# Optimization experiments

Hardware: AMD Instinct MI355X
Metric: run time of the kernel (lower is better)

## Reference

```python
import jax, jax.numpy as jnp
import numpy as np

B, S, HID = 2, 2048, 2048
H, HKV, D = 16, 8, 128
RQ, RK, RV = 6, 2, 2
WINDOW = 1024
SOFTCAP = 50.0
SCALING = D ** -0.5
NEG_INF = -2.3819763e38  # gemma mask fill value (fp32 safe)


def _rope(x, cos, sin):
    # Gemma rotary: split last dim into two halves treated as (real, imag).
    d2 = x.shape[-1] // 2
    x1, x2 = x[..., :d2], x[..., d2:]
    return jnp.concatenate([x1 * cos - x2 * sin, x1 * sin + x2 * cos], axis=-1)


def setup_inputs() -> dict:
    key = jax.random.key(0)
    ks = jax.random.split(key, 8)
    hidden_states = jax.random.normal(ks[0], (B, S, HID), jnp.float32)
    w = 0.02
    W_A_q = jax.random.normal(ks[1], (HID, H * RQ), jnp.float32) * w
    W_B_q = jax.random.normal(ks[2], (HID, H * RQ * D), jnp.float32) * w
    W_A_k = jax.random.normal(ks[3], (HID, HKV * RK), jnp.float32) * w
    W_B_k = jax.random.normal(ks[4], (HID, RK * D), jnp.float32) * w
    W_A_v = jax.random.normal(ks[5], (HID, HKV * RV), jnp.float32) * w
    W_B_v = jax.random.normal(ks[6], (HID, RV * D), jnp.float32) * w
    W_o = jax.random.normal(ks[7], (H * D, HID), jnp.float32) * w
    # rotary tables (theta=10000)
    pos = jnp.arange(S, dtype=jnp.float32)
    inv = 1.0 / (10000.0 ** (jnp.arange(0, D, 2, dtype=jnp.float32) / D))
    ang = pos[:, None] * inv[None, :]  # [S, D/2]
    freqs_cos, freqs_sin = jnp.cos(ang), jnp.sin(ang)
    # causal + sliding-window additive mask [B,1,S,S]
    i = jnp.arange(S)[:, None]
    j = jnp.arange(S)[None, :]
    allowed = (j <= i) & (i - j < WINDOW)
    mask = jnp.where(allowed, 0.0, NEG_INF).astype(jnp.float32)
    mask = jnp.broadcast_to(mask[None, None], (B, 1, S, S))
    kv_write_indices = jnp.arange(S, dtype=jnp.int32)  # prefill: identity write
    return {
        'hidden_states': hidden_states, 'W_A_q': W_A_q, 'W_B_q': W_B_q,
        'W_A_k': W_A_k, 'W_B_k': W_B_k, 'W_A_v': W_A_v, 'W_B_v': W_B_v,
        'W_o': W_o, 'freqs_cos': freqs_cos, 'freqs_sin': freqs_sin,
        'mask': mask, 'kv_write_indices': kv_write_indices,
    }


def reference(hidden_states, W_A_q, W_B_q, W_A_k, W_B_k, W_A_v, W_B_v, W_o,
              freqs_cos, freqs_sin, mask, kv_write_indices):
    # Prefill: kv_write_indices == arange(S); factorized cache == current factors.
    b, s, _ = hidden_states.shape
    Aq = (hidden_states @ W_A_q).reshape(b, s, H, RQ)       # [b,s,H,Rq]
    Bq = (hidden_states @ W_B_q).reshape(b, s, H, RQ, D)    # [b,s,H,Rq,d]
    Ak = (hidden_states @ W_A_k).reshape(b, s, HKV, RK)
    Bk = (hidden_states @ W_B_k).reshape(b, s, RK, D)
    Av = (hidden_states @ W_A_v).reshape(b, s, HKV, RV)
    Bv = (hidden_states @ W_B_v).reshape(b, s, RV, D)
    # RoPE on the B factors (as in the original: applied to B_q rows and B_k rows)
    Bq = _rope(Bq, freqs_cos[:, None, None, :], freqs_sin[:, None, None, :])
    Bk = _rope(Bk, freqs_cos[:, None, :], freqs_sin[:, None, :])
    # Contract rank factors. Identical math to the per-head
    # einsum('bqrd,bksd->bqkrs') + einsum('bqr,bks,bqkrs->bqk') since the
    # bilinear form factorizes: sum_{r,s} Aq_r Ak_s <Bq_r, Bk_s> = <q, k>.
    q = jnp.einsum('bshr,bshrd->bshd', Aq, Bq)               # [b,s,H,d]
    k = jnp.einsum('bsgr,bsrd->bsgd', Ak, Bk)                # [b,s,Hkv,d]
    v = jnp.einsum('bsgr,bsrd->bsgd', Av, Bv)
    rep = H // HKV
    k = jnp.repeat(k, rep, axis=2)                            # GQA expand
    v = jnp.repeat(v, rep, axis=2)
    scores = jnp.einsum('bqhd,bkhd->bhqk', q, k) * SCALING
    scores = jnp.tanh(scores / SOFTCAP) * SOFTCAP             # logit softcap
    scores = scores + mask                                    # local sliding mask
    probs = jax.nn.softmax(scores, axis=-1)
    out = jnp.einsum('bhqk,bkhd->bqhd', probs, v).reshape(b, s, H * D)
    return out @ W_o
```

## Files before the change

kernel.cpp:

```cpp
#include <hip/hip_runtime.h>
#include <hip/hip_bf16.h>

#define S_LEN 2048
#define HID 2048
#define NB 2
#define NH 16
#define NKV 8
#define DH 128
#define RQ 6
#define KG 2048
#define SCALING 0.08838834764831845f

typedef __attribute__((ext_vector_type(8))) short s16x8;
typedef __attribute__((ext_vector_type(4))) float f32x4;

__device__ __forceinline__ float bf2f(ushort u) {
    union { unsigned int i; float f; } v; v.i = ((unsigned int)u) << 16; return v.f;
}
__device__ __forceinline__ ushort f2bf(float f) {
    __hip_bfloat16 h = __float2bfloat16(f);
    return *reinterpret_cast<ushort*>(&h);
}
__device__ __forceinline__ void g2lds16(const void* g, void* l) {
    __builtin_amdgcn_global_load_lds((const __attribute__((address_space(1))) void*)g,
                                     (__attribute__((address_space(3))) void*)l, 16, 0, 0);
}

__global__ void k_prep(const float* __restrict__ hs, const float* __restrict__ WAq,
                       const float* __restrict__ WAk, const float* __restrict__ WAv,
                       const float* __restrict__ WBk, const float* __restrict__ WBv,
                       const float* __restrict__ WBq, const float* __restrict__ Wo,
                       ushort* __restrict__ Xb, ushort* __restrict__ WtS,
                       ushort* __restrict__ WtBq, ushort* __restrict__ WtWo) {
    __shared__ ushort tile[64][68];
    int idx = blockIdx.x;
    int t = threadIdx.x;
    if (idx < 2048) {
#pragma unroll
        for (int j = 0; j < 4; ++j) {
            int i = idx * 1024 + t + j * 256;
            float4 v = ((const float4*)hs)[i];
            ushort4 o;
            o.x = f2bf(v.x); o.y = f2bf(v.y); o.z = f2bf(v.z); o.w = f2bf(v.w);
            ((ushort4*)Xb)[i] = o;
        }
        return;
    }
    idx -= 2048;
    const float* in; ushort* out; int Nin, rowOff;
    if (idx < 64)        { in = WAq; out = WtS;  Nin = 96;    rowOff = 0; }
    else if (idx < 96)   { idx -= 64;   in = WAk; out = WtS;  Nin = 16;    rowOff = 96; }
    else if (idx < 128)  { idx -= 96;   in = WAv; out = WtS;  Nin = 16;    rowOff = 112; }
    else if (idx < 256)  { idx -= 128;  in = WBk; out = WtS;  Nin = 256;   rowOff = 128; }
    else if (idx < 384)  { idx -= 256;  in = WBv; out = WtS;  Nin = 256;   rowOff = 384; }
    else if (idx < 6528) { idx -= 384;  in = WBq; out = WtBq; Nin = 12288; rowOff = 0; }
    else                 { idx -= 6528; in = Wo;  out = WtWo; Nin = 2048;  rowOff = 0; }
    int k0 = (idx & 31) * 64, n0 = (idx >> 5) * 64;
#pragma unroll
    for (int i = 0; i < 4; ++i) {
        int f = t + i * 256;
        int r = f >> 4;
        int c = (f & 15) * 4;
        int nn = n0 + c;
        float4 v = make_float4(0.f, 0.f, 0.f, 0.f);
        if (nn < Nin) v = *(const float4*)&in[(size_t)(k0 + r) * Nin + nn];
        ushort4 u;
        u.x = f2bf(v.x); u.y = f2bf(v.y); u.z = f2bf(v.z); u.w = f2bf(v.w);
        *(ushort4*)&tile[r][c] = u;
    }
    __syncthreads();
#pragma unroll
    for (int i = 0; i < 4; ++i) {
        int f = t + i * 256;
        int nr = f >> 4;
        int kc = (f & 15) * 4;
        int nn = n0 + nr;
        if (nn < Nin) {
            ushort4 u;
            u.x = tile[kc][nr]; u.y = tile[kc + 1][nr];
            u.z = tile[kc + 2][nr]; u.w = tile[kc + 3][nr];
            *(ushort4*)&out[(size_t)(rowOff + nn) * KG + k0 + kc] = u;
        }
    }
}

__device__ __forceinline__ void stc(float* p, float v) { *p = v; }
__device__ __forceinline__ void stc(ushort* p, float v) { *p = f2bf(v); }

template<typename OutT>
__global__ __launch_bounds__(256, 2) void k_gemm(const ushort* __restrict__ A,
                                                 const ushort* __restrict__ Bt,
                                                 OutT* __restrict__ C, int ldc) {
    __shared__ ushort lA[128 * 64];
    __shared__ ushort lB[128 * 64];
    const int tid = threadIdx.x;
    const int l = tid & 63, w = tid >> 6;
    const int gx = gridDim.x;
    int flat = blockIdx.y * gx + blockIdx.x;
    const int nwg = gx * gridDim.y;
    if ((nwg & 7) == 0) {
        int qq = nwg >> 3;
        flat = (flat & 7) * qq + (flat >> 3);
    }
    const int m0 = (flat % gx) * 128, n0 = (flat / gx) * 128;
    const int wm = w >> 1, wn = w & 1;
    f32x4 acc[4][4] = {};
    const int swz = 16 * ((tid & 7) ^ ((tid >> 3) & 7));
    const int rowbase = tid >> 3;

    for (int k0 = 0; k0 < KG; k0 += 64) {
#pragma unroll
        for (int i = 0; i < 4; ++i) {
            int row = rowbase + i * 32;
            const char* srcA = (const char*)A + (((size_t)(m0 + row) * KG + k0) * 2) + swz;
            g2lds16(srcA, (char*)lA + tid * 16 + i * 4096);
            const char* srcB = (const char*)Bt + (((size_t)(n0 + row) * KG + k0) * 2) + swz;
            g2lds16(srcB, (char*)lB + tid * 16 + i * 4096);
        }
        __syncthreads();
#pragma unroll
        for (int kk = 0; kk < 2; ++kk) {
            s16x8 af[4], bfr[4];
            const int kb = kk * 64 + (l >> 4) * 16;
#pragma unroll
            for (int mf = 0; mf < 4; ++mf) {
                int row = wm * 64 + mf * 16 + (l & 15);
                af[mf] = *(const s16x8*)((const char*)lA + row * 128 + (kb ^ ((row & 7) << 4)));
            }
#pragma unroll
            for (int nf = 0; nf < 4; ++nf) {
                int row = wn * 64 + nf * 16 + (l & 15);
                bfr[nf] = *(const s16x8*)((const char*)lB + row * 128 + (kb ^ ((row & 7) << 4)));
            }
#pragma unroll
            for (int mf = 0; mf < 4; ++mf)
#pragma unroll
                for (int nf = 0; nf < 4; ++nf)
                    acc[mf][nf] = __builtin_amdgcn_mfma_f32_16x16x32_bf16(af[mf], bfr[nf], acc[mf][nf], 0, 0, 0);
        }
        __syncthreads();
    }
#pragma unroll
    for (int mf = 0; mf < 4; ++mf)
#pragma unroll
        for (int r = 0; r < 4; ++r) {
            int row = m0 + wm * 64 + mf * 16 + (l >> 4) * 4 + r;
#pragma unroll
            for (int nf = 0; nf < 4; ++nf) {
                int col = n0 + wn * 64 + nf * 16 + (l & 15);
                stc(C + (size_t)row * ldc + col, acc[mf][nf][r]);
            }
        }
}

__global__ __launch_bounds__(512, 2) void k_gemm8(const ushort* __restrict__ A,
                                                  const ushort* __restrict__ Bt,
                                                  ushort* __restrict__ C, int ldc) {
    __shared__ char sB[131072];
    const int tid = threadIdx.x;
    const int l = tid & 63, wid = tid >> 6;
    const int wr = wid >> 2, wc = wid & 3;

    int flat = blockIdx.x;
    const int nwg = gridDim.x;
    if ((nwg & 7) == 0) {
        int qq = nwg >> 3;
        flat = (flat & 7) * qq + (flat >> 3);
    }
    const int m0 = (flat & 15) * 256;
    const int n0 = (flat >> 4) * 256;

    const int rb = tid >> 3;
    const int swz = 16 * ((tid & 7) ^ (rb & 7));
    const char* pAh[2][2];
    const char* pBh[2][2];
#pragma unroll
    for (int h = 0; h < 2; ++h)
#pragma unroll
        for (int j = 0; j < 2; ++j) {
            pAh[h][j] = (const char*)A + (size_t)(m0 + j * 128 + h * 64 + rb) * (KG * 2) + swz;
            pBh[h][j] = (const char*)Bt + (size_t)(n0 + (j * 2 + (tid >> 8)) * 64 + h * 32 + (rb & 31)) * (KG * 2) + swz;
        }

    f32x4 acc[8][4] = {};
    s16x8 af[4][2], bf[4][2];

    const int arow = (l & 15) * 128;
    const int kxor0 = (0 * 64 + (l >> 4) * 16) ^ ((l & 7) << 4);
    const int kxor1 = (1 * 64 + (l >> 4) * 16) ^ ((l & 7) << 4);

#define STG_A(T, D, H)                                                                     \
    do {                                                                                   \
        g2lds16(pAh[H][0] + (size_t)(T) * 128, sB + (D) * 65536 + (H) * 16384 + tid * 16); \
        g2lds16(pAh[H][1] + (size_t)(T) * 128, sB + (D) * 65536 + (H) * 16384 + 8192 + tid * 16); \
    } while (0)
#define STG_B(T, D, H)                                                                     \
    do {                                                                                   \
        g2lds16(pBh[H][0] + (size_t)(T) * 128, sB + (D) * 65536 + 32768 + (H) * 16384 + tid * 16); \
        g2lds16(pBh[H][1] + (size_t)(T) * 128, sB + (D) * 65536 + 32768 + (H) * 16384 + 8192 + tid * 16); \
    } while (0)
#define RD_A(D, MH)                                                                        \
    do {                                                                                   \
        const char* ab = sB + (D) * 65536 + (MH) * 16384 + wr * 8192;                      \
        _Pragma("unroll") for (int mi = 0; mi < 4; ++mi) {                                 \
            af[mi][0] = *(const s16x8*)(ab + mi * 2048 + arow + kxor0);                    \
            af[mi][1] = *(const s16x8*)(ab + mi * 2048 + arow + kxor1);                    \
        }                                                                                  \
    } while (0)
#define RD_B(D, BH)                                                                        \
    do {                                                                                   \
        const char* bb = sB + (D) * 65536 + 32768 + (BH) * 16384 + wc * 4096;              \
        _Pragma("unroll") for (int ni = 0; ni < 2; ++ni) {                                 \
            bf[(BH) * 2 + ni][0] = *(const s16x8*)(bb + ni * 2048 + arow + kxor0);         \
            bf[(BH) * 2 + ni][1] = *(const s16x8*)(bb + ni * 2048 + arow + kxor1);         \
        }                                                                                  \
    } while (0)
#define QMFMA(MQ, NQ)                                                                      \
    do {                                                                                   \
        __builtin_amdgcn_s_setprio(1);                                                     \
        _Pragma("unroll") for (int mi = 0; mi < 4; ++mi)                                   \
        _Pragma("unroll") for (int ni = 0; ni < 2; ++ni)                                   \
        _Pragma("unroll") for (int k2 = 0; k2 < 2; ++k2)                                   \
            acc[(MQ) * 4 + mi][(NQ) * 2 + ni] = __builtin_amdgcn_mfma_f32_16x16x32_bf16(   \
                af[mi][k2], bf[(NQ) * 2 + ni][k2], acc[(MQ) * 4 + mi][(NQ) * 2 + ni], 0, 0, 0); \
        __builtin_amdgcn_s_setprio(0);                                                     \
    } while (0)
#define BAR()                                   \
    do {                                        \
        asm volatile("" ::: "memory");          \
        __builtin_amdgcn_s_barrier();           \
        asm volatile("" ::: "memory");          \
    } while (0)
#define VM6() asm volatile("s_waitcnt vmcnt(6)" ::: "memory")
#define VM0() asm volatile("s_waitcnt vmcnt(0)" ::: "memory")

    STG_A(0, 0, 0); STG_A(0, 0, 1); STG_B(0, 0, 0); STG_B(0, 0, 1);
    STG_B(1, 1, 0); STG_B(1, 1, 1); STG_A(1, 1, 0);
    VM6();
    BAR();

    for (int i = 0; i < 16; ++i) {
        const bool last = (i == 15);
        const int t1 = 2 * i + 1, t2 = 2 * i + 2, t3 = 2 * i + 3;
        RD_A(0, 0); RD_B(0, 0);
        STG_A(t1, 1, 1);
        BAR(); QMFMA(0, 0); BAR();
        RD_B(0, 1);
        if (!last) STG_A(t2, 0, 0);
        BAR(); QMFMA(0, 1); BAR();
        RD_A(0, 1);
        if (!last) STG_B(t2, 0, 0);
        BAR(); QMFMA(1, 1); BAR();
        if (!last) { STG_B(t2, 0, 1); VM6(); } else { VM0(); }
        BAR(); QMFMA(1, 0); BAR();
        RD_A(1, 0); RD_B(1, 0);
        if (!last) STG_A(t2, 0, 1);
        BAR(); QMFMA(0, 0); BAR();
        RD_B(1, 1);
        if (!last) STG_B(t3, 1, 0);
        BAR(); QMFMA(0, 1); BAR();
        RD_A(1, 1);
        if (!last) STG_B(t3, 1, 1);
        BAR(); QMFMA(1, 1); BAR();
        if (!last) { STG_A(t3, 1, 0); VM6(); }
        BAR(); QMFMA(1, 0); BAR();
    }

#undef STG_A
#undef STG_B
#undef RD_A
#undef RD_B
#undef QMFMA

#pragma unroll
    for (int mf = 0; mf < 8; ++mf)
#pragma unroll
        for (int r = 0; r < 4; ++r) {
            int row = m0 + wr * 128 + mf * 16 + (l >> 4) * 4 + r;
#pragma unroll
            for (int nf = 0; nf < 4; ++nf) {
                int col = n0 + wc * 64 + nf * 16 + (l & 15);
                C[(size_t)row * ldc + col] = f2bf(acc[mf][nf][r]);
            }
        }
#undef BAR
#undef VM6
#undef VM0
}

__global__ __launch_bounds__(512, 2) void k_gemm8h(const ushort* __restrict__ A,
                                                   const ushort* __restrict__ Bt,
                                                   float* __restrict__ C, int ldc) {
    __shared__ char sB[98304];
    const int tid = threadIdx.x;
    const int l = tid & 63, wid = tid >> 6;
    const int wr = wid >> 2, wc = wid & 3;

    int flat = blockIdx.x;
    const int nwg = gridDim.x;
    if ((nwg & 7) == 0) {
        int qq = nwg >> 3;
        flat = (flat & 7) * qq + (flat >> 3);
    }
    const int m0 = (flat & 31) * 128;
    const int n0 = (flat >> 5) * 256;

    const int rb = tid >> 3;
    const int swz = 16 * ((tid & 7) ^ (rb & 7));
    const char* pA_[2];
    const char* pB_[2][2];
#pragma unroll
    for (int h = 0; h < 2; ++h) {
        pA_[h] = (const char*)A + (size_t)(m0 + (tid >> 8) * 64 + h * 32 + (rb & 31)) * (KG * 2) + swz;
#pragma unroll
        for (int j = 0; j < 2; ++j)
            pB_[h][j] = (const char*)Bt + (size_t)(n0 + (j * 2 + (tid >> 8)) * 64 + h * 32 + (rb & 31)) * (KG * 2) + swz;
    }

    f32x4 acc[4][4] = {};
    s16x8 af[2][2], bf[4][2];

    const int arow = (l & 15) * 128;
    const int kxor0 = ((l >> 4) * 16) ^ ((l & 7) << 4);
    const int kxor1 = (64 + (l >> 4) * 16) ^ ((l & 7) << 4);

#define STG_AH(T, D, H)                                                                    \
    g2lds16(pA_[H] + (size_t)(T) * 128, sB + (D) * 49152 + (H) * 8192 + tid * 16)
#define STG_BH(T, D, H)                                                                    \
    do {                                                                                   \
        g2lds16(pB_[H][0] + (size_t)(T) * 128, sB + (D) * 49152 + 16384 + (H) * 16384 + tid * 16); \
        g2lds16(pB_[H][1] + (size_t)(T) * 128, sB + (D) * 49152 + 16384 + (H) * 16384 + 8192 + tid * 16); \
    } while (0)
#define RD_AH(D, MH)                                                                       \
    do {                                                                                   \
        const char* ab = sB + (D) * 49152 + (MH) * 8192 + wr * 4096;                       \
        _Pragma("unroll") for (int mi = 0; mi < 2; ++mi) {                                 \
            af[mi][0] = *(const s16x8*)(ab + mi * 2048 + arow + kxor0);                    \
            af[mi][1] = *(const s16x8*)(ab + mi * 2048 + arow + kxor1);                    \
        }                                                                                  \
    } while (0)
#define RD_BH(D, BH)                                                                       \
    do {                                                                                   \
        const char* bb = sB + (D) * 49152 + 16384 + (BH) * 16384 + wc * 4096;              \
        _Pragma("unroll") for (int ni = 0; ni < 2; ++ni) {                                 \
            bf[(BH) * 2 + ni][0] = *(const s16x8*)(bb + ni * 2048 + arow + kxor0);         \
            bf[(BH) * 2 + ni][1] = *(const s16x8*)(bb + ni * 2048 + arow + kxor1);         \
        }                                                                                  \
    } while (0)
#define QMFMAH(MQ, NQ)                                                                     \
    do {                                                                                   \
        __builtin_amdgcn_s_setprio(1);                                                     \
        _Pragma("unroll") for (int mi = 0; mi < 2; ++mi)                                   \
        _Pragma("unroll") for (int ni = 0; ni < 2; ++ni)                                   \
        _Pragma("unroll") for (int k2 = 0; k2 < 2; ++k2)                                   \
            acc[(MQ) * 2 + mi][(NQ) * 2 + ni] = __builtin_amdgcn_mfma_f32_16x16x32_bf16(   \
                af[mi][k2], bf[(NQ) * 2 + ni][k2], acc[(MQ) * 2 + mi][(NQ) * 2 + ni], 0, 0, 0); \
        __builtin_amdgcn_s_setprio(0);                                                     \
    } while (0)
#define BAR()                                   \
    do {                                        \
        asm volatile("" ::: "memory");          \
        __builtin_amdgcn_s_barrier();           \
        asm volatile("" ::: "memory");          \
    } while (0)
#define VM5() asm volatile("s_waitcnt vmcnt(5)" ::: "memory")
#define VM0() asm volatile("s_waitcnt vmcnt(0)" ::: "memory")

    STG_AH(0, 0, 0); STG_AH(0, 0, 1); STG_BH(0, 0, 0); STG_BH(0, 0, 1);
    STG_BH(1, 1, 0); STG_BH(1, 1, 1); STG_AH(1, 1, 0);
    VM5();
    BAR();

    for (int i = 0; i < 16; ++i) {
        const bool last = (i == 15);
        const int t1 = 2 * i + 1, t2 = 2 * i + 2, t3 = 2 * i + 3;
        RD_AH(0, 0); RD_BH(0, 0);
        STG_AH(t1, 1, 1);
        BAR(); QMFMAH(0, 0); BAR();
        RD_BH(0, 1);
        if (!last) STG_AH(t2, 0, 0);
        BAR(); QMFMAH(0, 1); BAR();
        RD_AH(0, 1);
        if (!last) STG_BH(t2, 0, 0);
        BAR(); QMFMAH(1, 1); BAR();
        if (!last) { STG_BH(t2, 0, 1); VM5(); } else { VM0(); }
        BAR(); QMFMAH(1, 0); BAR();
        RD_AH(1, 0); RD_BH(1, 0);
        if (!last) STG_AH(t2, 0, 1);
        BAR(); QMFMAH(0, 0); BAR();
        RD_BH(1, 1);
        if (!last) STG_BH(t3, 1, 0);
        BAR(); QMFMAH(0, 1); BAR();
        RD_AH(1, 1);
        if (!last) STG_BH(t3, 1, 1);
        BAR(); QMFMAH(1, 1); BAR();
        if (!last) { STG_AH(t3, 1, 0); VM5(); }
        BAR(); QMFMAH(1, 0); BAR();
    }

#undef STG_AH
#undef STG_BH
#undef RD_AH
#undef RD_BH
#undef QMFMAH
#undef BAR
#undef VM5
#undef VM0

#pragma unroll
    for (int a = 0; a < 4; ++a)
#pragma unroll
        for (int r = 0; r < 4; ++r) {
            int row = m0 + wr * 64 + a * 16 + (l >> 4) * 4 + r;
#pragma unroll
            for (int b2 = 0; b2 < 4; ++b2) {
                int col = n0 + wc * 64 + b2 * 16 + (l & 15);
                C[(size_t)row * ldc + col] = acc[a][b2][r];
            }
        }
}

__global__ void k_contract_q(const ushort* __restrict__ bq, const float* __restrict__ small,
                             const float* __restrict__ cosT, const float* __restrict__ sinT,
                             ushort* __restrict__ q, int pitch, int hbase) {
    int srow = blockIdx.x;
    int b = srow >> 11, sl = srow & 2047;
    int t = threadIdx.x;
    int l = t & 63;
    int hloc = blockIdx.y * 4 + (t >> 6);
    int h = hbase + hloc;
    const ushort* bqr = bq + (size_t)srow * pitch + hloc * 768;
    const float* af = small + (size_t)srow * 640 + h * RQ;
    float y0 = 0.f, y1 = 0.f;
#pragma unroll
    for (int r = 0; r < RQ; ++r) {
        float a = af[r];
        ushort2 v = *(const ushort2*)&bqr[r * 128 + 2 * l];
        y0 += a * bf2f(v.x);
        y1 += a * bf2f(v.y);
    }
    float z0 = __shfl_xor(y0, 32);
    float z1 = __shfl_xor(y1, 32);
    int d = (l & 31) * 2;
    float2 cs = *(const float2*)&cosT[sl * 64 + d];
    float2 sn = *(const float2*)&sinT[sl * 64 + d];
    size_t o = ((size_t)(b * NH + h) * S_LEN + sl) * DH;
    ushort2 outv;
    if (l < 32) {
        outv.x = f2bf((y0 * cs.x - z0 * sn.x) * SCALING);
        outv.y = f2bf((y1 * cs.y - z1 * sn.y) * SCALING);
        *(ushort2*)&q[o + d] = outv;
    } else {
        outv.x = f2bf((z0 * sn.x + y0 * cs.x) * SCALING);
        outv.y = f2bf((z1 * sn.y + y1 * cs.y) * SCALING);
        *(ushort2*)&q[o + 64 + d] = outv;
    }
}

__global__ void k_contract_kv(const float* __restrict__ small, const float* __restrict__ cosT,
                              const float* __restrict__ sinT, ushort* __restrict__ kk,
                              ushort* __restrict__ vT) {
    int srow = blockIdx.x;
    int b = srow >> 11, sl = srow & 2047;
    int t = threadIdx.x;
    int d2 = t & 63, g = t >> 6;
    const float* row = small + (size_t)srow * 640;
    float k1 = 0.f, k2 = 0.f, v1 = 0.f, v2 = 0.f;
#pragma unroll
    for (int r = 0; r < 2; ++r) {
        float ak = row[96 + g * 2 + r];
        k1 += ak * row[128 + r * 128 + d2];
        k2 += ak * row[128 + r * 128 + 64 + d2];
        float av = row[112 + g * 2 + r];
        v1 += av * row[384 + r * 128 + d2];
        v2 += av * row[384 + r * 128 + 64 + d2];
    }
    float c = cosT[sl * 64 + d2], s = sinT[sl * 64 + d2];
    float kr1 = k1 * c - k2 * s, kr2 = k1 * s + k2 * c;
    size_t ko = ((size_t)(b * NKV + g) * S_LEN + sl) * DH + d2;
    kk[ko] = f2bf(kr1);
    kk[ko + 64] = f2bf(kr2);
    size_t vo = ((size_t)(b * NKV + g) * DH + d2) * S_LEN + sl;
    vT[vo] = f2bf(v1);
    vT[vo + (size_t)64 * S_LEN] = f2bf(v2);
}

__device__ __forceinline__ float softcap_p(float x) {
    float z = x * 0.02f;
    float z2 = z * z;
    float num = z * fmaf(z2, z2 + 105.f, 945.f);
    float den = fmaf(z2, fmaf(z2, 15.f, 420.f), 945.f);
    return __expf(fmaf(50.f, __fdividef(num, den), -50.f));
}

template<int FUSEQ>
__global__ __launch_bounds__(512, 2) void k_attn(const ushort* __restrict__ qsrc,
                                                 const float* __restrict__ small,
                                                 const float* __restrict__ cosT,
                                                 const float* __restrict__ sinT,
                                                 const ushort* __restrict__ kk,
                                                 const ushort* __restrict__ vT,
                                                 ushort* __restrict__ O) {
    __shared__ char sK[2][16384];
    __shared__ char sV[2][16384];
    __shared__ char sP[16384];
    const int f = blockIdx.x;
    const int xcd = f & 7;
    const int j = f >> 3;
    const int bg = xcd * 2 + (j >> 5);
    const int qb = 31 - (j & 31);
    const int b = bg >> 3, g = bg & 7;
    const int tid = threadIdx.x, l = tid & 63, w = tid >> 6;
    const int w4 = w & 3;
    const int h = g * 2 + (w >> 2);
    const int qs = qb * 64;
    const int q0 = qs + w4 * 16;

    s16x8 qf[4];
    if (FUSEQ) {
        const int row = q0 + (l & 15);
        const int srow = b * S_LEN + row;
        const float* af = small + (size_t)srow * 640 + h * RQ;
        const ushort* bqr = qsrc + (size_t)srow * 12288 + h * 768;
        const int k8 = (l >> 4) * 8;
#pragma unroll
        for (int grp = 0; grp < 2; ++grp) {
            const int dbase = grp * 32 + k8;
            float x1[8] = {}, x2[8] = {};
#pragma unroll
            for (int r = 0; r < RQ; ++r) {
                float a = af[r];
                s16x8 v1 = *(const s16x8*)&bqr[r * 128 + dbase];
                s16x8 v2 = *(const s16x8*)&bqr[r * 128 + 64 + dbase];
#pragma unroll
                for (int e = 0; e < 8; ++e) {
                    x1[e] = fmaf(a, bf2f((ushort)v1[e]), x1[e]);
                    x2[e] = fmaf(a, bf2f((ushort)v2[e]), x2[e]);
                }
            }
            const float* cp = &cosT[row * 64 + dbase];
            const float* sp = &sinT[row * 64 + dbase];
            s16x8 lo, hi;
#pragma unroll
            for (int e = 0; e < 8; ++e) {
                float c = cp[e], s = sp[e];
                lo[e] = (short)f2bf((x1[e] * c - x2[e] * s) * SCALING);
                hi[e] = (short)f2bf((x1[e] * s + x2[e] * c) * SCALING);
            }
            qf[grp] = lo;
            qf[grp + 2] = hi;
        }
    } else {
        const ushort* qbase = qsrc + ((size_t)(b * NH + h) * S_LEN) * DH;
        const char* qrow = (const char*)(qbase + (size_t)(q0 + (l & 15)) * DH);
#pragma unroll
        for (int ds = 0; ds < 4; ++ds)
            qf[ds] = *(const s16x8*)(qrow + ds * 64 + (l >> 4) * 16);
    }

    f32x4 acc[8] = {};
    float lrow[4] = {0.f, 0.f, 0.f, 0.f};

    const size_t kgbase = ((size_t)(b * NKV + g) * S_LEN) * DH * 2;
    const size_t vgbase = ((size_t)(b * NKV + g) * DH) * S_LEN * 2;

    const int jt0 = (qs > 1023) ? ((qs - 1023) >> 6) : 0;
    const int ibase = q0 + (l >> 4) * 4;

    const int krow0 = tid >> 4, kcolb = (tid & 15) * 16;
    const int vrow0 = tid >> 3, vcolb = (tid & 7) * 16;

#define STAGE_KV(JT, SLOT)                                                                   \
    do {                                                                                     \
        _Pragma("unroll")                                                                    \
        for (int i = 0; i < 2; ++i) {                                                        \
            int row = krow0 + i * 32;                                                        \
            const char* src = (const char*)kk + kgbase + ((size_t)((JT) * 64 + row)) * 256   \
                              + (kcolb ^ ((row & 7) << 4));                                  \
            g2lds16(src, &sK[SLOT][tid * 16 + i * 8192]);                                    \
        }                                                                                    \
        _Pragma("unroll")                                                                    \
        for (int i = 0; i < 2; ++i) {                                                        \
            int row = vrow0 + i * 64;                                                        \
            const char* src = (const char*)vT + vgbase + (size_t)row * 4096                  \
                              + (size_t)(JT) * 128 + (vcolb ^ ((row & 7) << 4));             \
            g2lds16(src, &sV[SLOT][tid * 16 + i * 8192]);                                    \
        }                                                                                    \
    } while (0)

    STAGE_KV(jt0, 0);
    asm volatile("s_waitcnt vmcnt(0)" ::: "memory");
    __builtin_amdgcn_s_barrier();
    asm volatile("" ::: "memory");

    for (int jt = jt0; jt <= qb; ++jt) {
        const int cur = (jt - jt0) & 1;
        if (jt < qb) STAGE_KV(jt + 1, cur ^ 1);

        const bool diag = (jt == qb);
        const bool wclip = (jt == jt0) && (qs > 1023);

        f32x4 sc[4] = {};
#pragma unroll
        for (int ct = 0; ct < 4; ++ct) {
            if (diag && ct > w4) continue;
            f32x4 z = {};
            int row = ct * 16 + (l & 15);
#pragma unroll
            for (int ds = 0; ds < 4; ++ds) {
                int kb = ds * 64 + (l >> 4) * 16;
                s16x8 kf = *(const s16x8*)(&sK[cur][row * 256 + (kb ^ ((row & 7) << 4))]);
                z = __builtin_amdgcn_mfma_f32_16x16x32_bf16(qf[ds], kf, z, 0, 0, 0);
            }
            sc[ct] = z;
        }
        float p[4][4];
        if (!diag && !wclip) {
#pragma unroll
            for (int ct = 0; ct < 4; ++ct)
#pragma unroll
                for (int r = 0; r < 4; ++r) {
                    float pe = softcap_p(sc[ct][r]);
                    p[ct][r] = pe;
                    lrow[r] += pe;
                }
        } else if (diag) {
#pragma unroll
            for (int ct = 0; ct < 4; ++ct) {
                if (ct > w4) {
#pragma unroll
                    for (int r = 0; r < 4; ++r) p[ct][r] = 0.f;
                    continue;
                }
                int j2 = jt * 64 + ct * 16 + (l & 15);
#pragma unroll
                for (int r = 0; r < 4; ++r) {
                    float pe = softcap_p(sc[ct][r]);
                    pe = (j2 <= ibase + r) ? pe : 0.f;
                    p[ct][r] = pe;
                    lrow[r] += pe;
                }
            }
        } else {
#pragma unroll
            for (int ct = 0; ct < 4; ++ct) {
                int j2 = jt * 64 + ct * 16 + (l & 15);
#pragma unroll
                for (int r = 0; r < 4; ++r) {
                    float pe = softcap_p(sc[ct][r]);
                    pe = (j2 > ibase + r - 1024) ? pe : 0.f;
                    p[ct][r] = pe;
                    lrow[r] += pe;
                }
            }
        }
#pragma unroll
        for (int ct = 0; ct < 4; ++ct) {
            int col = ct * 16 + (l & 15);
#pragma unroll
            for (int r = 0; r < 4; ++r) {
                int row = (l >> 4) * 4 + r;
                *(ushort*)(sP + w * 2048 + row * 128 + ((col * 2) ^ ((row & 7) << 4))) = f2bf(p[ct][r]);
            }
        }
#pragma unroll
        for (int s2 = 0; s2 < 2; ++s2) {
            int rowp = l & 15;
            int kb = s2 * 64 + (l >> 4) * 16;
            s16x8 pf = *(const s16x8*)(sP + w * 2048 + rowp * 128 + (kb ^ ((rowp & 7) << 4)));
#pragma unroll
            for (int dt = 0; dt < 8; ++dt) {
                int d = dt * 16 + (l & 15);
                s16x8 vf = *(const s16x8*)(&sV[cur][d * 128 + (kb ^ ((d & 7) << 4))]);
                acc[dt] = __builtin_amdgcn_mfma_f32_16x16x32_bf16(pf, vf, acc[dt], 0, 0, 0);
            }
        }

        asm volatile("s_waitcnt vmcnt(0)" ::: "memory");
        __builtin_amdgcn_s_barrier();
        asm volatile("" ::: "memory");
    }
#undef STAGE_KV

#pragma unroll
    for (int r = 0; r < 4; ++r) {
        float rs = lrow[r];
        rs += __shfl_xor(rs, 1); rs += __shfl_xor(rs, 2);
        rs += __shfl_xor(rs, 4); rs += __shfl_xor(rs, 8);
        lrow[r] = rs;
    }
#pragma unroll
    for (int r = 0; r < 4; ++r) {
        int row = qs + w4 * 16 + (l >> 4) * 4 + r;
        float inv = 1.f / lrow[r];
#pragma unroll
        for (int dt = 0; dt < 8; ++dt)
            O[((size_t)(b * S_LEN + row)) * HID + h * DH + dt * 16 + (l & 15)] = f2bf(acc[dt][r] * inv);
    }
}

extern "C" void kernel_launch(void* const* d_in, const int* in_sizes, int n_in,
                              void* d_out, int out_size, void* d_ws, size_t ws_size,
                              hipStream_t stream) {
    (void)in_sizes; (void)n_in; (void)out_size;
    const float* hs  = (const float*)d_in[0];
    const float* WAq = (const float*)d_in[1];
    const float* WBq = (const float*)d_in[2];
    const float* WAk = (const float*)d_in[3];
    const float* WBk = (const float*)d_in[4];
    const float* WAv = (const float*)d_in[5];
    const float* WBv = (const float*)d_in[6];
    const float* Wo  = (const float*)d_in[7];
    const float* fc  = (const float*)d_in[8];
    const float* fs  = (const float*)d_in[9];

    char* ws = (char*)d_ws;
    ushort* Xb    = (ushort*)(ws + 0);
    ushort* WtS   = (ushort*)(ws + 16777216);
    ushort* WtBq  = (ushort*)(ws + 19398656);
    ushort* WtWo  = (ushort*)(ws + 69730304);
    float*  Small = (float*) (ws + 78118912);
    ushort* BqC   = (ushort*)(ws + 88604672);

    const bool bigws = (ws_size >= 239599616ull);
    size_t tail = bigws ? 189267968ull : 113770496ull;
    ushort* qB  = (ushort*)(ws + tail);
    ushort* kB  = (ushort*)(ws + tail + 16777216);
    ushort* vTB = (ushort*)(ws + tail + 25165824);
    ushort* OB  = (ushort*)(ws + tail + 33554432);

    k_prep<<<9600, 256, 0, stream>>>(hs, WAq, WAk, WAv, WBk, WBv, WBq, Wo,
                                     Xb, WtS, WtBq, WtWo);

    k_gemm<float><<<dim3(32, 5), 256, 0, stream>>>(Xb, WtS, Small, 640);
    k_contract_kv<<<4096, 512, 0, stream>>>(Small, fc, fs, kB, vTB);

    if (bigws) {
        k_gemm8<<<768, 512, 0, stream>>>(Xb, WtBq, BqC, 12288);
        k_attn<1><<<512, 512, 0, stream>>>(BqC, Small, fc, fs, kB, vTB, OB);
    } else {
        for (int c = 0; c < 4; ++c) {
            k_gemm8<<<192, 512, 0, stream>>>(Xb, WtBq + (size_t)c * 3072 * KG, BqC, 3072);
            k_contract_q<<<dim3(4096, 1), 256, 0, stream>>>(BqC, Small, fc, fs, qB, 3072, c * 4);
        }
        k_attn<0><<<512, 512, 0, stream>>>(qB, Small, fc, fs, kB, vTB, OB);
    }

    k_gemm8h<<<256, 512, 0, stream>>>(OB, WtWo, (float*)d_out, 2048);
}
```

Baseline: 421.3 us.

## Merge small A-factor GEMM into big Bq GEMM launch as extra blocks

Creates a combined kernel whose first 768 blocks run the large Bq-factor GEMM and whose remaining 160 blocks run the small rank-factor GEMM writing Small. This replaces two separate launches in the big-workspace path, letting the small GEMM fill idle CUs alongside the large one and removing a launch plus its tail. k_contract_kv is moved after the merged launch. The small-GEMM blocks use the 512-thread launch with only 4 waves computing, wasting half the block's waves and sharing the large kernel's LDS/occupancy limits.

Result: no change. 418.9 us (-0.6%).

```diff
diff --git a/kernel.cpp b/kernel.cpp
--- a/kernel.cpp
+++ b/kernel.cpp
@@ -151,6 +151,211 @@
                 stc(C + (size_t)row * ldc + col, acc[mf][nf][r]);
             }
         }
+}
+
+__global__ __launch_bounds__(512, 2) void k_mega(const ushort* __restrict__ Xb,
+                                                 const ushort* __restrict__ WtBq,
+                                                 ushort* __restrict__ BqC,
+                                                 const ushort* __restrict__ WtS,
+                                                 float* __restrict__ Small) {
+    __shared__ char sB[131072];
+    const int tid = threadIdx.x;
+    const int l = tid & 63, wid = tid >> 6;
+
+    if (blockIdx.x < 768) {
+        const ushort* A = Xb;
+        const ushort* Bt = WtBq;
+        ushort* C = BqC;
+        const int ldc = 12288;
+        const int wr = wid >> 2, wc = wid & 3;
+
+        int flat = blockIdx.x;
+        {
+            int qq = 768 >> 3;
+            flat = (flat & 7) * qq + (flat >> 3);
+        }
+        const int m0 = (flat & 15) * 256;
+        const int n0 = (flat >> 4) * 256;
+
+        const int rb = tid >> 3;
+        const int swz = 16 * ((tid & 7) ^ (rb & 7));
+        const char* pAh[2][2];
+        const char* pBh[2][2];
+#pragma unroll
+        for (int h = 0; h < 2; ++h)
+#pragma unroll
+            for (int j = 0; j < 2; ++j) {
+                pAh[h][j] = (const char*)A + (size_t)(m0 + j * 128 + h * 64 + rb) * (KG * 2) + swz;
+                pBh[h][j] = (const char*)Bt + (size_t)(n0 + (j * 2 + (tid >> 8)) * 64 + h * 32 + (rb & 31)) * (KG * 2) + swz;
+            }
+
+        f32x4 acc[8][4] = {};
+        s16x8 af[4][2], bf[4][2];
+
+        const int arow = (l & 15) * 128;
+        const int kxor0 = (0 * 64 + (l >> 4) * 16) ^ ((l & 7) << 4);
+        const int kxor1 = (1 * 64 + (l >> 4) * 16) ^ ((l & 7) << 4);
+
+#define STG_A(T, D, H)                                                                     \
+    do {                                                                                   \
+        g2lds16(pAh[H][0] + (size_t)(T) * 128, sB + (D) * 65536 + (H) * 16384 + tid * 16); \
+        g2lds16(pAh[H][1] + (size_t)(T) * 128, sB + (D) * 65536 + (H) * 16384 + 8192 + tid * 16); \
+    } while (0)
+#define STG_B(T, D, H)                                                                     \
+    do {                                                                                   \
+        g2lds16(pBh[H][0] + (size_t)(T) * 128, sB + (D) * 65536 + 32768 + (H) * 16384 + tid * 16); \
+        g2lds16(pBh[H][1] + (size_t)(T) * 128, sB + (D) * 65536 + 32768 + (H) * 16384 + 8192 + tid * 16); \
+    } while (0)
+#define RD_A(D, MH)                                                                        \
+    do {                                                                                   \
+        const char* ab = sB + (D) * 65536 + (MH) * 16384 + wr * 8192;                      \
+        _Pragma("unroll") for (int mi = 0; mi < 4; ++mi) {                                 \
+            af[mi][0] = *(const s16x8*)(ab + mi * 2048 + arow + kxor0);                    \
+            af[mi][1] = *(const s16x8*)(ab + mi * 2048 + arow + kxor1);                    \
+        }                                                                                  \
+    } while (0)
+#define RD_B(D, BH)                                                                        \
+    do {                                                                                   \
+        const char* bb = sB + (D) * 65536 + 32768 + (BH) * 16384 + wc * 4096;              \
+        _Pragma("unroll") for (int ni = 0; ni < 2; ++ni) {                                 \
+            bf[(BH) * 2 + ni][0] = *(const s16x8*)(bb + ni * 2048 + arow + kxor0);         \
+            bf[(BH) * 2 + ni][1] = *(const s16x8*)(bb + ni * 2048 + arow + kxor1);         \
+        }                                                                                  \
+    } while (0)
+#define QMFMA(MQ, NQ)                                                                      \
+    do {                                                                                   \
+        __builtin_amdgcn_s_setprio(1);                                                     \
+        _Pragma("unroll") for (int mi = 0; mi < 4; ++mi)                                   \
+        _Pragma("unroll") for (int ni = 0; ni < 2; ++ni)                                   \
+        _Pragma("unroll") for (int k2 = 0; k2 < 2; ++k2)                                   \
+            acc[(MQ) * 4 + mi][(NQ) * 2 + ni] = __builtin_amdgcn_mfma_f32_16x16x32_bf16(   \
+                af[mi][k2], bf[(NQ) * 2 + ni][k2], acc[(MQ) * 4 + mi][(NQ) * 2 + ni], 0, 0, 0); \
+        __builtin_amdgcn_s_setprio(0);                                                     \
+    } while (0)
+#define BAR()                                   \
+    do {                                        \
+        asm volatile("" ::: "memory");          \
+        __builtin_amdgcn_s_barrier();           \
+        asm volatile("" ::: "memory");          \
+    } while (0)
+#define VM6() asm volatile("s_waitcnt vmcnt(6)" ::: "memory")
+#define VM0() asm volatile("s_waitcnt vmcnt(0)" ::: "memory")
+
+        STG_A(0, 0, 0); STG_A(0, 0, 1); STG_B(0, 0, 0); STG_B(0, 0, 1);
+        STG_B(1, 1, 0); STG_B(1, 1, 1); STG_A(1, 1, 0);
+        VM6();
+        BAR();
+
+        for (int i = 0; i < 16; ++i) {
+            const bool last = (i == 15);
+            const int t1 = 2 * i + 1, t2 = 2 * i + 2, t3 = 2 * i + 3;
+            RD_A(0, 0); RD_B(0, 0);
+            STG_A(t1, 1, 1);
+            BAR(); QMFMA(0, 0); BAR();
+            RD_B(0, 1);
+            if (!last) STG_A(t2, 0, 0);
+            BAR(); QMFMA(0, 1); BAR();
+            RD_A(0, 1);
+            if (!last) STG_B(t2, 0, 0);
+            BAR(); QMFMA(1, 1); BAR();
+            if (!last) { STG_B(t2, 0, 1); VM6(); } else { VM0(); }
+            BAR(); QMFMA(1, 0); BAR();
+            RD_A(1, 0); RD_B(1, 0);
+            if (!last) STG_A(t2, 0, 1);
+            BAR(); QMFMA(0, 0); BAR();
+            RD_B(1, 1);
+            if (!last) STG_B(t3, 1, 0);
+            BAR(); QMFMA(0, 1); BAR();
+            RD_A(1, 1);
+            if (!last) STG_B(t3, 1, 1);
+            BAR(); QMFMA(1, 1); BAR();
+            if (!last) { STG_A(t3, 1, 0); VM6(); }
+            BAR(); QMFMA(1, 0); BAR();
+        }
+
+#undef STG_A
+#undef STG_B
+#undef RD_A
+#undef RD_B
+#undef QMFMA
+#undef BAR
+#undef VM6
+#undef VM0
+
+#pragma unroll
+        for (int mf = 0; mf < 8; ++mf)
+#pragma unroll
+            for (int r = 0; r < 4; ++r) {
+                int row = m0 + wr * 128 + mf * 16 + (l >> 4) * 4 + r;
+#pragma unroll
+                for (int nf = 0; nf < 4; ++nf) {
+                    int col = n0 + wc * 64 + nf * 16 + (l & 15);
+                    C[(size_t)row * ldc + col] = f2bf(acc[mf][nf][r]);
+                }
+            }
+    } else {
+        ushort* lA = (ushort*)sB;
+        ushort* lB = (ushort*)(sB + 16384);
+        int flat = blockIdx.x - 768;
+        {
+            int qq = 160 >> 3;
+            flat = (flat & 7) * qq + (flat >> 3);
+        }
+        const int m0 = (flat % 32) * 128, n0 = (flat / 32) * 128;
+        const int w = wid;
+        const int wm = (w & 3) >> 1, wn = w & 1;
+        f32x4 acc[4][4] = {};
+        const int swz = 16 * ((tid & 7) ^ ((tid >> 3) & 7));
+        const int rowbase = tid >> 3;
+
+        for (int k0 = 0; k0 < KG; k0 += 64) {
+#pragma unroll
+            for (int i = 0; i < 2; ++i) {
+                int row = rowbase + i * 64;
+                const char* srcA = (const char*)Xb + (((size_t)(m0 + row) * KG + k0) * 2) + swz;
+                g2lds16(srcA, (char*)lA + tid * 16 + i * 8192);
+                const char* srcB = (const char*)WtS + (((size_t)(n0 + row) * KG + k0) * 2) + swz;
+                g2lds16(srcB, (char*)lB + tid * 16 + i * 8192);
+            }
+            __syncthreads();
+            if (w < 4) {
+#pragma unroll
+                for (int kk = 0; kk < 2; ++kk) {
+                    s16x8 af[4], bfr[4];
+                    const int kb = kk * 64 + (l >> 4) * 16;
+#pragma unroll
+                    for (int mf = 0; mf < 4; ++mf) {
+                        int row = wm * 64 + mf * 16 + (l & 15);
+                        af[mf] = *(const s16x8*)((const char*)lA + row * 128 + (kb ^ ((row & 7) << 4)));
+                    }
+#pragma unroll
+                    for (int nf = 0; nf < 4; ++nf) {
+                        int row = wn * 64 + nf * 16 + (l & 15);
+                        bfr[nf] = *(const s16x8*)((const char*)lB + row * 128 + (kb ^ ((row & 7) << 4)));
+                    }
+#pragma unroll
+                    for (int mf = 0; mf < 4; ++mf)
+#pragma unroll
+                        for (int nf = 0; nf < 4; ++nf)
+                            acc[mf][nf] = __builtin_amdgcn_mfma_f32_16x16x32_bf16(af[mf], bfr[nf], acc[mf][nf], 0, 0, 0);
+                }
+            }
+            __syncthreads();
+        }
+        if (w < 4) {
+#pragma unroll
+            for (int mf = 0; mf < 4; ++mf)
+#pragma unroll
+                for (int r = 0; r < 4; ++r) {
+                    int row = m0 + wm * 64 + mf * 16 + (l >> 4) * 4 + r;
+#pragma unroll
+                    for (int nf = 0; nf < 4; ++nf) {
+                        int col = n0 + wn * 64 + nf * 16 + (l & 15);
+                        Small[(size_t)row * 640 + col] = acc[mf][nf][r];
+                    }
+                }
+        }
+    }
 }
 
 __global__ __launch_bounds__(512, 2) void k_gemm8(const ushort* __restrict__ A,
@@ -732,13 +937,13 @@
     k_prep<<<9600, 256, 0, stream>>>(hs, WAq, WAk, WAv, WBk, WBv, WBq, Wo,
                                      Xb, WtS, WtBq, WtWo);
 
-    k_gemm<float><<<dim3(32, 5), 256, 0, stream>>>(Xb, WtS, Small, 640);
-    k_contract_kv<<<4096, 512, 0, stream>>>(Small, fc, fs, kB, vTB);
-
     if (bigws) {
-        k_gemm8<<<768, 512, 0, stream>>>(Xb, WtBq, BqC, 12288);
+        k_mega<<<928, 512, 0, stream>>>(Xb, WtBq, BqC, WtS, Small);
+        k_contract_kv<<<4096, 512, 0, stream>>>(Small, fc, fs, kB, vTB);
         k_attn<1><<<512, 512, 0, stream>>>(BqC, Small, fc, fs, kB, vTB, OB);
     } else {
+        k_gemm<float><<<dim3(32, 5), 256, 0, stream>>>(Xb, WtS, Small, 640);
+        k_contract_kv<<<4096, 512, 0, stream>>>(Small, fc, fs, kB, vTB);
         for (int c = 0; c < 4; ++c) {
             k_gemm8<<<192, 512, 0, stream>>>(Xb, WtBq + (size_t)c * 3072 * KG, BqC, 3072);
             k_contract_q<<<dim3(4096, 1), 256, 0, stream>>>(BqC, Small, fc, fs, qB, 3072, c * 4);
```
